# Kernel tuning notes

Measured on AMD Instinct MI355X. Metric: run time of the kernel, lower is better.

Reference implementation:

```python
import jax, jax.numpy as jnp
import numpy as np

FIXED_SIZE = 10
NUM_GRAPHS = 2000
NUM_PERM = 1


def setup_inputs() -> dict:
    key = jax.random.key(0)
    ks = jax.random.split(key, 8)
    N, E, D, H, O = 100000, 600000, 128, 256, 256
    x = jax.random.normal(ks[0], (N, D), dtype=jnp.float32)
    edge_index = jax.random.randint(ks[1], (2, E), 0, N)
    batch_ids = jnp.sort(jax.random.randint(ks[2], (N,), 0, NUM_GRAPHS))
    W1 = jax.random.normal(ks[3], (D + FIXED_SIZE, H), dtype=jnp.float32) * 0.05
    b1 = jnp.zeros((H,), dtype=jnp.float32)
    W2 = jax.random.normal(ks[4], (H, O), dtype=jnp.float32) * 0.05
    b2 = jnp.zeros((O,), dtype=jnp.float32)
    return {"x": x, "edge_index": edge_index, "batch_ids": batch_ids,
            "W1": W1, "b1": b1, "W2": W2, "b2": b2}


def _gnn(new_x, src, dst, W1, b1, W2, b2):
    # 2-layer GIN-style sum-aggregation node embedder
    N = new_x.shape[0]
    m = jax.ops.segment_sum(new_x[src], dst, num_segments=N)
    h = jax.nn.relu((new_x + m) @ W1 + b1)
    m = jax.ops.segment_sum(h[src], dst, num_segments=N)
    h = jax.nn.relu((h + m) @ W2 + b2)
    return h


def reference(x, edge_index, batch_ids, W1, b1, W2, b2):
    N = x.shape[0]
    src, dst = edge_index[0], edge_index[1]
    # segment starts (batch_ids is sorted)
    counts = jax.ops.segment_sum(jnp.ones((N,), jnp.int32), batch_ids, num_segments=NUM_GRAPHS)
    starts = jnp.cumsum(counts) - counts  # [G]
    perm_key = jax.random.key(42)
    out = None
    for p in range(NUM_PERM):
        # vectorized per-graph random permutation: sort random keys within each segment
        r = jax.random.uniform(jax.random.fold_in(perm_key, p), (N,))
        order = jnp.argsort(batch_ids.astype(jnp.float32) + r)  # groups by graph, random within
        # rank within graph after permutation (order preserves segment boundaries)
        ranks = jnp.zeros((N,), jnp.int32).at[order].set(
            jnp.arange(N, dtype=jnp.int32) - starts[batch_ids].astype(jnp.int32))
        # tiled eye(10) indexed by permuted position == one-hot of (rank % 10)
        ids = jax.nn.one_hot(ranks % FIXED_SIZE, FIXED_SIZE, dtype=x.dtype)
        new_x = jnp.concatenate([x, ids], axis=1)  # [N, D+10]
        h_v = _gnn(new_x, src, dst, W1, b1, W2, b2)
        h_g = jax.ops.segment_sum(h_v, batch_ids, num_segments=NUM_GRAPHS)  # global_add_pool
        contrib = h_g / NUM_PERM
        out = contrib if out is None else out + contrib
    return out
```

## Files before the change

kernel.cpp:

```cpp
#include <hip/hip_runtime.h>
#include <hip/hip_bf16.h>
#include <stdint.h>


#define D_IN   128
#define KRAW   138
#define K1     160
#define B1ROW  192
#define HDIM   256
#define NGRAPH 2000
#define MAXS   6

typedef __bf16 bf16x8 __attribute__((ext_vector_type(8)));
typedef float  f32x4  __attribute__((ext_vector_type(4)));

__device__ __forceinline__ unsigned short f2b(float f) {
  __hip_bfloat16 h = __float2bfloat16(f);
  return __builtin_bit_cast(unsigned short, h);
}
__device__ __forceinline__ float blo(unsigned p) { return __uint_as_float(p << 16); }
__device__ __forceinline__ float bhi(unsigned p) { return __uint_as_float(p & 0xffff0000u); }

__device__ __forceinline__ unsigned e8(float f) {
  unsigned u = __float_as_uint(f);
  unsigned s = (u >> 24) & 0x80u;
  float a = fabsf(f);
  if (!(a >= 0.015625f)) return s;
  a = fminf(a, 448.f);
  unsigned b = __float_as_uint(a);
  b += 0x0007FFFFu + ((b >> 20) & 1u);
  unsigned e = (b >> 23) - 120u;
  unsigned m = (b >> 20) & 7u;
  return s | (e << 3) | m;
}
__device__ __forceinline__ float d8(unsigned byte) {
  unsigned m = byte & 0x7fu;
  unsigned bits = (0x3C000000u + (m << 20)) | ((byte & 0x80u) << 24);
  return m ? __uint_as_float(bits) : 0.f;
}

__device__ __forceinline__ void glds16(const unsigned short* g, unsigned short* l) {
  __builtin_amdgcn_global_load_lds(
      (const __attribute__((address_space(1))) unsigned int*)g,
      (__attribute__((address_space(3))) unsigned int*)l, 16, 0, 0);
}

__device__ __forceinline__ unsigned rotl32(unsigned x, int r) {
  return (x << r) | (x >> (32 - r));
}
__device__ __forceinline__ void threefry2x32(unsigned k0, unsigned k1,
                                             unsigned x0, unsigned x1,
                                             unsigned& o0, unsigned& o1) {
  unsigned ks2 = k0 ^ k1 ^ 0x1BD11BDAu;
  unsigned ks[3] = {k0, k1, ks2};
  x0 += ks[0]; x1 += ks[1];
  const int rotA[4] = {13, 15, 26, 6};
  const int rotB[4] = {17, 29, 16, 24};
#pragma unroll
  for (int i = 0; i < 5; ++i) {
    const int* rot = (i & 1) ? rotB : rotA;
#pragma unroll
    for (int j = 0; j < 4; ++j) {
      x0 += x1; x1 = rotl32(x1, rot[j]); x1 ^= x0;
    }
    x0 += ks[(i + 1) % 3];
    x1 += ks[(i + 2) % 3] + (unsigned)(i + 1);
  }
  o0 = x0; o1 = x1;
}

__global__ void k_prep2(const int* __restrict__ bids, const int* __restrict__ dst,
                        float* __restrict__ r, int* __restrict__ start,
                        int* __restrict__ cnt, int* __restrict__ deg, int N, int E) {
  int i = blockIdx.x * blockDim.x + threadIdx.x;
  if (i < E) atomicAdd(&deg[dst[i]], 1);
  if (i >= N) return;
  int half = N >> 1;
  if (i < half) {
    unsigned fk0, fk1;
    threefry2x32(0u, 42u, 0u, 0u, fk0, fk1);
    unsigned b0, b1v;
    threefry2x32(fk0, fk1, (unsigned)i, (unsigned)(i + half), b0, b1v);
    r[i]        = __uint_as_float((b0  >> 9) | 0x3f800000u) - 1.0f;
    r[i + half] = __uint_as_float((b1v >> 9) | 0x3f800000u) - 1.0f;
  }
  int g = bids[i];
  if (i == 0 || bids[i - 1] != g) start[g] = i;
  atomicAdd(&cnt[g], 1);
}

__global__ void k_rank(const float* __restrict__ r, const int* __restrict__ start,
                       const int* __restrict__ cnt, int* __restrict__ ids) {
  int g = blockIdx.x;
  int st = start[g], n = cnt[g];
  if (n <= 0) return;
  float gf = (float)g;
  for (int t = threadIdx.x; t < n; t += blockDim.x) {
    int v = st + t;
    float kv = gf + r[v];
    int c = 0;
    for (int u0 = 0; u0 < n; ++u0) {
      int u = st + u0;
      float ku = gf + r[u];
      c += (int)((ku < kv) | ((ku == kv) & (u < v)));
    }
    ids[v] = c % 10;
  }
}

__global__ void k_scan1(const int* __restrict__ deg, int* __restrict__ rowptr,
                        int* __restrict__ bsum, int N) {
  __shared__ int buf[256];
  int tid = threadIdx.x;
  int i = blockIdx.x * 256 + tid;
  int v = (i < N) ? deg[i] : 0;
  buf[tid] = v;
  __syncthreads();
  for (int off = 1; off < 256; off <<= 1) {
    int t = (tid >= off) ? buf[tid - off] : 0;
    __syncthreads();
    buf[tid] += t;
    __syncthreads();
  }
  if (i < N) rowptr[i] = buf[tid] - v;
  if (tid == 255) bsum[blockIdx.x] = buf[255];
}

__global__ void k_scan2(int* __restrict__ bsum, int nb) {
  __shared__ int buf[512];
  int tid = threadIdx.x;
  int v = (tid < nb) ? bsum[tid] : 0;
  buf[tid] = v;
  __syncthreads();
  for (int off = 1; off < 512; off <<= 1) {
    int t = (tid >= off) ? buf[tid - off] : 0;
    __syncthreads();
    buf[tid] += t;
    __syncthreads();
  }
  if (tid < nb) bsum[tid] = buf[tid] - v;
}

__global__ void k_scan3(int* __restrict__ rowptr, const int* __restrict__ bsum,
                        int N, int E) {
  int i = blockIdx.x * 256 + threadIdx.x;
  if (i < N) rowptr[i] += bsum[blockIdx.x];
  if (i == 0) rowptr[N] = E;
}

__global__ void k_scatter(const int* __restrict__ src, const int* __restrict__ dst,
                          const int* __restrict__ rowptr, int* __restrict__ fill,
                          int* __restrict__ csr, int E) {
  int e = blockIdx.x * 256 + threadIdx.x;
  if (e >= E) return;
  int d = dst[e];
  int pos = rowptr[d] + atomicAdd(&fill[d], 1);
  csr[pos] = src[e];
}

__global__ void k_pre(const float* __restrict__ x, const float* __restrict__ W1,
                      const float* __restrict__ W2, unsigned char* __restrict__ x8,
                      unsigned short* __restrict__ Wpt, unsigned short* __restrict__ W2t,
                      int n8, int xbb) {
  int bid = blockIdx.x;
  int tid = threadIdx.x;
  if (bid < xbb) {
    int i = bid * 256 + tid;
    if (i >= n8) return;
    const float4* xp = reinterpret_cast<const float4*>(x) + (size_t)i * 2;
    float4 v0 = xp[0], v1 = xp[1];
    uint2 o;
    o.x = e8(v0.x) | (e8(v0.y) << 8) | (e8(v0.z) << 16) | (e8(v0.w) << 24);
    o.y = e8(v1.x) | (e8(v1.y) << 8) | (e8(v1.z) << 16) | (e8(v1.w) << 24);
    reinterpret_cast<uint2*>(x8)[i] = o;
  } else {
    int j = (bid - xbb) * 256 + tid;
    if (j < HDIM * B1ROW) {
      int n = j / B1ROW, k = j % B1ROW;
      Wpt[j] = f2b(k < KRAW ? W1[k * HDIM + n] : 0.f);
    } else {
      int j2 = j - HDIM * B1ROW;
      if (j2 < HDIM * HDIM) {
        int n = j2 >> 8, k = j2 & 255;
        W2t[j2] = f2b(W2[k * HDIM + n]);
      }
    }
  }
}

__global__ void k_agg1(const unsigned char* __restrict__ x8, const int* __restrict__ ids,
                       const int* __restrict__ rowptr, const int* __restrict__ csr,
                       unsigned short* __restrict__ agg1, int N) {
  int v = blockIdx.x * 4 + (threadIdx.x >> 6);
  if (v >= N) return;
  int l = threadIdx.x & 63;
  const unsigned short* xbase = reinterpret_cast<const unsigned short*>(x8);
  unsigned t = xbase[(size_t)v * 64 + l];
  float a0 = d8(t & 0xffu), a1 = d8(t >> 8);
  int e0 = rowptr[v], e1 = rowptr[v + 1];
  int e = e0;
  for (; e + 4 <= e1; e += 4) {
    unsigned t0 = xbase[(size_t)csr[e] * 64 + l];
    unsigned t1 = xbase[(size_t)csr[e + 1] * 64 + l];
    unsigned t2 = xbase[(size_t)csr[e + 2] * 64 + l];
    unsigned t3 = xbase[(size_t)csr[e + 3] * 64 + l];
    a0 += d8(t0 & 0xffu) + d8(t1 & 0xffu) + d8(t2 & 0xffu) + d8(t3 & 0xffu);
    a1 += d8(t0 >> 8) + d8(t1 >> 8) + d8(t2 >> 8) + d8(t3 >> 8);
  }
  for (; e < e1; ++e) {
    unsigned tt = xbase[(size_t)csr[e] * 64 + l];
    a0 += d8(tt & 0xffu); a1 += d8(tt >> 8);
  }
  int cnt10[10] = {};
  for (int base = e0; base < e1; base += 64) {
    int ee = base + l;
    int id = (ee < e1) ? ids[csr[ee]] : -1;
#pragma unroll
    for (int k = 0; k < 10; ++k)
      cnt10[k] += (int)__popcll(__ballot(id == k));
  }
  int myid = ids[v];
  unsigned* row32 = reinterpret_cast<unsigned*>(agg1 + (size_t)v * K1);
  row32[l] = (unsigned)f2b(a0) | ((unsigned)f2b(a1) << 16);
  if (l < 16) {
    float v0 = 0.f, v1 = 0.f;
#pragma unroll
    for (int kk = 0; kk < 10; ++kk) {
      float cv = (float)(cnt10[kk] + (myid == kk ? 1 : 0));
      if (2 * l == kk) v0 = cv;
      if (2 * l + 1 == kk) v1 = cv;
    }
    row32[64 + l] = (unsigned)f2b(v0) | ((unsigned)f2b(v1) << 16);
  }
}

template <int KT, int BROW, int NT, int EPI>
__global__ __launch_bounds__(512, 1) void k_gemm(
    const unsigned short* __restrict__ A, const unsigned short* __restrict__ Bt,
    const float* __restrict__ bias, void* __restrict__ Hout, int M) {
  constexpr int ROWB = BROW * 2;
  __shared__ __align__(16) unsigned short b_s[HDIM * BROW];
  __shared__ __align__(16) unsigned short a_s[3 * 4096];

  const int tid = threadIdx.x;
  const int w = tid >> 6, l = tid & 63;
  const int wm = w >> 2, wn = w & 3;
  const int lr = l & 15, lq = l >> 4, lk = lq * 8;
  const int b = blockIdx.x;
  const int TT = (M + 127) >> 7;
  const int ntb = (TT > b) ? ((TT - b + 255) >> 8) : 0;
  const int total = ntb * NT;

  constexpr int BITERS = BROW / 16;
#pragma unroll
  for (int it = 0; it < BITERS; ++it) {
    int d = (it * 512 + tid) * 16;
    int n = d / ROWB;
    int inrow = d - n * ROWB;
    int u = inrow ^ ((n & 7) << 4);
    glds16(Bt + (size_t)n * BROW + (u >> 1), b_s + (size_t)(it * 512 + w * 64) * 8);
  }
  auto stageA = [&](int s) {
    int buf = s - (s / 3) * 3;
    int m0 = (b + (s / NT) * 256) << 7;
    int k0 = (s % NT) * 32;
    int d = tid * 16;
    int u = d ^ (((d >> 7) & 7) << 4);
    int r = ((u >> 7) << 1) | ((u >> 6) & 1);
    int k = (u >> 1) & 31;
    glds16(A + (size_t)(m0 + r) * KT + k0 + k, a_s + buf * 4096 + w * 512);
  };
  if (total > 0) stageA(0);
  if (total > 1) stageA(1);
  if (total > 1) { asm volatile("s_waitcnt vmcnt(1)" ::: "memory"); }
  else           { asm volatile("s_waitcnt vmcnt(0)" ::: "memory"); }
  __builtin_amdgcn_s_barrier();
  __builtin_amdgcn_sched_barrier(0);

  float bv[4];
  if constexpr (EPI == 0) {
#pragma unroll
    for (int nf = 0; nf < 4; ++nf) bv[nf] = bias[wn * 64 + nf * 16 + lr];
  }

  int aoff[4];
#pragma unroll
  for (int mf = 0; mf < 4; ++mf) {
    int R = wm * 64 + mf * 16 + lr;
    aoff[mf] = (((R >> 1) * 128 + (R & 1) * 64 + lk * 2) ^ (((R >> 1) & 7) << 4));
  }

  int s = 0;
  for (int ti = 0; ti < ntb; ++ti) {
    const int m0t = (b + ti * 256) << 7;
    f32x4 acc[4][4] = {};
    for (int ks = 0; ks < NT; ++ks, ++s) {
      const bool pre = (s + 2 < total);
      if (pre) stageA(s + 2);
      const char* ab = reinterpret_cast<const char*>(a_s) + (s - (s / 3) * 3) * 8192;
      bf16x8 af[4], bfr[4];
#pragma unroll
      for (int mf = 0; mf < 4; ++mf)
        af[mf] = *reinterpret_cast<const bf16x8*>(ab + aoff[mf]);
#pragma unroll
      for (int nf = 0; nf < 4; ++nf) {
        int n = wn * 64 + nf * 16 + lr;
        int bb = n * ROWB + (((ks * 32 + lk) * 2) ^ ((n & 7) << 4));
        bfr[nf] = *reinterpret_cast<const bf16x8*>(reinterpret_cast<const char*>(b_s) + bb);
      }
      __builtin_amdgcn_s_setprio(1);
#pragma unroll
      for (int mf = 0; mf < 4; ++mf)
#pragma unroll
        for (int nf = 0; nf < 4; ++nf)
          acc[mf][nf] = __builtin_amdgcn_mfma_f32_16x16x32_bf16(af[mf], bfr[nf], acc[mf][nf], 0, 0, 0);
      __builtin_amdgcn_s_setprio(0);
      if (pre) { asm volatile("s_waitcnt vmcnt(1)" ::: "memory"); }
      else     { asm volatile("s_waitcnt vmcnt(0)" ::: "memory"); }
      __builtin_amdgcn_s_barrier();
      __builtin_amdgcn_sched_barrier(0);
    }

#pragma unroll
    for (int mf = 0; mf < 4; ++mf)
#pragma unroll
      for (int q = 0; q < 4; ++q) {
        int grow = m0t + wm * 64 + mf * 16 + lq * 4 + q;
        if (grow < M) {
          size_t ro = (size_t)grow * HDIM + wn * 64 + lr;
          if constexpr (EPI == 0) {
            unsigned short* H = (unsigned short*)Hout;
#pragma unroll
            for (int nf = 0; nf < 4; ++nf) {
              float vv = acc[mf][nf][q] + bv[nf];
              H[ro + nf * 16] = f2b(vv > 0.f ? vv : 0.f);
            }
          } else {
            unsigned char* H8 = (unsigned char*)Hout;
#pragma unroll
            for (int nf = 0; nf < 4; ++nf)
              H8[ro + nf * 16] = (unsigned char)e8(acc[mf][nf][q]);
          }
        }
      }
  }
}

__global__ __launch_bounds__(256) void k_gp(
    const unsigned char* __restrict__ y8, const int* __restrict__ bids,
    const int* __restrict__ rowptr, const int* __restrict__ csr,
    const float* __restrict__ b2, float* __restrict__ out, int N) {
  __shared__ float red[4][MAXS][HDIM];
  __shared__ int seg_l[128];
  __shared__ int gseg_l[128];
  __shared__ int wtot2[2];
  __shared__ int nseg_sh;
  const int tid = threadIdx.x;
  const int w = tid >> 6, l = tid & 63;
  const int v0 = blockIdx.x * 128;

  float* rz = &red[0][0][0];
  for (int i = tid; i < 4 * MAXS * HDIM; i += 256) rz[i] = 0.f;

  if (tid < 128) {
    int i0 = v0 + tid; i0 = i0 < N ? i0 : N - 1;
    int i1 = v0 + tid - 1; i1 = i1 < N ? i1 : N - 1; i1 = i1 > 0 ? i1 : 0;
    int g = bids[i0];
    bool bnd = (tid > 0) && (g != bids[i1]);
    unsigned long long mb = __ballot(bnd);
    int lane = tid & 63;
    int incl = (int)__popcll(mb & (~0ULL >> (63 - lane)));
    seg_l[tid] = incl;
    if (lane == 63) wtot2[tid >> 6] = incl;
  }
  __syncthreads();
  if (tid < 128) {
    int sfin = seg_l[tid] + ((tid >= 64) ? wtot2[0] : 0);
    seg_l[tid] = sfin;
    int i0 = v0 + tid; i0 = i0 < N ? i0 : N - 1;
    int i1 = v0 + tid - 1; i1 = i1 < N ? i1 : N - 1; i1 = i1 > 0 ? i1 : 0;
    int g = bids[i0];
    if (tid == 0 || g != bids[i1]) gseg_l[sfin] = g;
    if (tid == 127) nseg_sh = sfin + 1;
  }
  __syncthreads();
  const int nseg = nseg_sh;
  const bool fb = (nseg > MAXS);

  float bv0 = b2[l * 4 + 0], bv1 = b2[l * 4 + 1];
  float bv2 = b2[l * 4 + 2], bv3 = b2[l * 4 + 3];
  const unsigned* yb = reinterpret_cast<const unsigned*>(y8);

  float a0 = 0.f, a1 = 0.f, a2 = 0.f, a3 = 0.f;
  int cur = seg_l[w * 32];
  for (int i = 0; i < 32; ++i) {
    int idx = w * 32 + i;
    int v = v0 + idx;
    if (v >= N) break;
    int sg = seg_l[idx];
    if (sg != cur) {
      if (!fb) {
        float* rp = &red[w][cur][l * 4];
        rp[0] += a0; rp[1] += a1; rp[2] += a2; rp[3] += a3;
      }
      a0 = a1 = a2 = a3 = 0.f;
      cur = sg;
    }
    unsigned t = yb[(size_t)v * 64 + l];
    float s0 = d8(t & 0xffu), s1 = d8((t >> 8) & 0xffu);
    float s2 = d8((t >> 16) & 0xffu), s3 = d8(t >> 24);
    int e0 = rowptr[v], e1 = rowptr[v + 1];
    int e = e0;
    for (; e + 4 <= e1; e += 4) {
      unsigned t0 = yb[(size_t)csr[e] * 64 + l];
      unsigned t1 = yb[(size_t)csr[e + 1] * 64 + l];
      unsigned t2 = yb[(size_t)csr[e + 2] * 64 + l];
      unsigned t3 = yb[(size_t)csr[e + 3] * 64 + l];
      s0 += d8(t0 & 0xffu) + d8(t1 & 0xffu) + d8(t2 & 0xffu) + d8(t3 & 0xffu);
      s1 += d8((t0 >> 8) & 0xffu) + d8((t1 >> 8) & 0xffu) + d8((t2 >> 8) & 0xffu) + d8((t3 >> 8) & 0xffu);
      s2 += d8((t0 >> 16) & 0xffu) + d8((t1 >> 16) & 0xffu) + d8((t2 >> 16) & 0xffu) + d8((t3 >> 16) & 0xffu);
      s3 += d8(t0 >> 24) + d8(t1 >> 24) + d8(t2 >> 24) + d8(t3 >> 24);
    }
    for (; e < e1; ++e) {
      unsigned tt = yb[(size_t)csr[e] * 64 + l];
      s0 += d8(tt & 0xffu); s1 += d8((tt >> 8) & 0xffu);
      s2 += d8((tt >> 16) & 0xffu); s3 += d8(tt >> 24);
    }
    s0 = fmaxf(s0 + bv0, 0.f); s1 = fmaxf(s1 + bv1, 0.f);
    s2 = fmaxf(s2 + bv2, 0.f); s3 = fmaxf(s3 + bv3, 0.f);
    if (fb) {
      int g = bids[v];
      float* op = out + (size_t)g * HDIM + l * 4;
      if (s0 > 0.f) atomicAdd(&op[0], s0);
      if (s1 > 0.f) atomicAdd(&op[1], s1);
      if (s2 > 0.f) atomicAdd(&op[2], s2);
      if (s3 > 0.f) atomicAdd(&op[3], s3);
    } else {
      a0 += s0; a1 += s1; a2 += s2; a3 += s3;
    }
  }
  if (!fb) {
    float* rp = &red[w][cur][l * 4];
    rp[0] += a0; rp[1] += a1; rp[2] += a2; rp[3] += a3;
  }
  __syncthreads();
  if (!fb) {
    for (int sg = 0; sg < nseg; ++sg) {
      float val = red[0][sg][tid] + red[1][sg][tid] + red[2][sg][tid] + red[3][sg][tid];
      if (val != 0.f) atomicAdd(&out[(size_t)gseg_l[sg] * HDIM + tid], val);
    }
  }
}

extern "C" void kernel_launch(void* const* d_in, const int* in_sizes, int n_in,
                              void* d_out, int out_size, void* d_ws, size_t ws_size,
                              hipStream_t stream) {
  const float* x    = (const float*)d_in[0];
  const int*   ei   = (const int*)d_in[1];
  const int*   bids = (const int*)d_in[2];
  const float* W1   = (const float*)d_in[3];
  const float* b1   = (const float*)d_in[4];
  const float* W2   = (const float*)d_in[5];
  const float* b2   = (const float*)d_in[6];
  float* out = (float*)d_out;

  const int N = in_sizes[2];
  const int E = in_sizes[1] / 2;
  const int* src = ei;
  const int* dst = ei + E;

  char* ws = (char*)d_ws;
  size_t off = 0;
  auto alloc = [&](size_t bytes) {
    size_t o = off;
    off = (off + bytes + 255) & ~(size_t)255;
    return o;
  };
  float* r      = (float*)(ws + alloc((size_t)N * 4));
  int*   ids    = (int*)(ws + alloc((size_t)N * 4));
  int*   start  = (int*)(ws + alloc((size_t)NGRAPH * 4));
  int*   cnt    = (int*)(ws + alloc((size_t)NGRAPH * 4));
  int*   deg    = (int*)(ws + alloc((size_t)N * 4));
  int*   fill   = (int*)(ws + alloc((size_t)N * 4));
  int*   rowptr = (int*)(ws + alloc((size_t)(N + 1) * 4));
  int*   bsum   = (int*)(ws + alloc(512 * 4));
  int*   csr    = (int*)(ws + alloc((size_t)E * 4));
  unsigned short* Wpt = (unsigned short*)(ws + alloc((size_t)HDIM * B1ROW * 2));
  unsigned short* W2t = (unsigned short*)(ws + alloc((size_t)HDIM * HDIM * 2));
  unsigned char*  x8  = (unsigned char*)(ws + alloc((size_t)N * D_IN));
  unsigned short* agg1 = (unsigned short*)(ws + alloc((size_t)(N + 128) * K1 * 2));
  unsigned short* h    = (unsigned short*)(ws + alloc((size_t)(N + 128) * HDIM * 2));
  unsigned char*  y8   = (unsigned char*)(ws + alloc((size_t)(N + 128) * HDIM));
  (void)ws_size;

  size_t zspan = (size_t)((char*)(fill + N) - (char*)cnt);
  hipMemsetAsync(cnt, 0, zspan, stream);
  hipMemsetAsync(out, 0, (size_t)out_size * 4, stream);

  const int nb = (N + 255) / 256;
  const int n8 = N * 16;
  const int xbb = (n8 + 255) / 256;
  const int wb = (HDIM * B1ROW + HDIM * HDIM + 255) / 256;

  k_prep2<<<(E + 255) / 256, 256, 0, stream>>>(bids, dst, r, start, cnt, deg, N, E);
  k_pre<<<xbb + wb, 256, 0, stream>>>(x, W1, W2, x8, Wpt, W2t, n8, xbb);
  k_scan1<<<nb, 256, 0, stream>>>(deg, rowptr, bsum, N);
  k_scan2<<<1, 512, 0, stream>>>(bsum, nb);
  k_scan3<<<nb, 256, 0, stream>>>(rowptr, bsum, N, E);
  k_scatter<<<(E + 255) / 256, 256, 0, stream>>>(src, dst, rowptr, fill, csr, E);
  k_rank<<<NGRAPH, 64, 0, stream>>>(r, start, cnt, ids);
  k_agg1<<<(N + 3) / 4, 256, 0, stream>>>(x8, ids, rowptr, csr, agg1, N);

  k_gemm<K1, B1ROW, 5, 0><<<256, 512, 0, stream>>>(agg1, Wpt, b1, (void*)h, N);
  k_gemm<HDIM, HDIM, 8, 1><<<256, 512, 0, stream>>>(h, W2t, nullptr, (void*)y8, N);

  k_gp<<<(N + 127) / 128, 256, 0, stream>>>(y8, bids, rowptr, csr, b2, out, N);
}
```

Before: 423.7 us.

## Use hardware FP8 pack/unpack and simplify graph pooling to per-wave atomics

Replaces the software e4m3 encode/decode routines with the packed hardware FP8 conversion builtins when available, in input quantization, the first aggregation, the second GEMM epilogue and the final aggregation. The final aggregate+pool kernel is restructured so each wave processes 8 consecutive nodes and flushes per-graph partial sums directly with global atomics. This drops the shared-memory segment scan and reduction buffers and their barriers. In exchange it issues more global atomics, and it depends on the hardware FP8 format matching the software codec.

```diff
diff --git a/kernel.cpp b/kernel.cpp
--- a/kernel.cpp
+++ b/kernel.cpp
@@ -9,19 +9,21 @@
 #define B1ROW  192
 #define HDIM   256
 #define NGRAPH 2000
-#define MAXS   6
 
 typedef __bf16 bf16x8 __attribute__((ext_vector_type(8)));
 typedef float  f32x4  __attribute__((ext_vector_type(4)));
+typedef float  f32x2  __attribute__((ext_vector_type(2)));
 
 __device__ __forceinline__ unsigned short f2b(float f) {
   __hip_bfloat16 h = __float2bfloat16(f);
   return __builtin_bit_cast(unsigned short, h);
 }
-__device__ __forceinline__ float blo(unsigned p) { return __uint_as_float(p << 16); }
-__device__ __forceinline__ float bhi(unsigned p) { return __uint_as_float(p & 0xffff0000u); }
-
-__device__ __forceinline__ unsigned e8(float f) {
+
+#if __has_builtin(__builtin_amdgcn_cvt_pk_f32_fp8) && __has_builtin(__builtin_amdgcn_cvt_pk_fp8_f32)
+#define HW_FP8 1
+#endif
+
+__device__ __forceinline__ unsigned e8_sw(float f) {
   unsigned u = __float_as_uint(f);
   unsigned s = (u >> 24) & 0x80u;
   float a = fabsf(f);
@@ -33,10 +35,36 @@
   unsigned m = (b >> 20) & 7u;
   return s | (e << 3) | m;
 }
-__device__ __forceinline__ float d8(unsigned byte) {
+__device__ __forceinline__ float d8_sw(unsigned byte) {
   unsigned m = byte & 0x7fu;
   unsigned bits = (0x3C000000u + (m << 20)) | ((byte & 0x80u) << 24);
   return m ? __uint_as_float(bits) : 0.f;
+}
+
+template <bool HI>
+__device__ __forceinline__ f32x2 dec2(unsigned w) {
+#ifdef HW_FP8
+  return __builtin_amdgcn_cvt_pk_f32_fp8((int)w, HI);
+#else
+  unsigned hw = HI ? (w >> 16) : (w & 0xffffu);
+  f32x2 r; r.x = d8_sw(hw & 0xffu); r.y = d8_sw(hw >> 8); return r;
+#endif
+}
+template <bool HI>
+__device__ __forceinline__ int enc2(float a, float b, int old) {
+#ifdef HW_FP8
+  return __builtin_amdgcn_cvt_pk_fp8_f32(a, b, old, HI);
+#else
+  unsigned p = e8_sw(a) | (e8_sw(b) << 8);
+  return HI ? ((old & 0xffff) | (int)(p << 16)) : ((int)(old & 0xffff0000u) | (int)p);
+#endif
+}
+__device__ __forceinline__ unsigned char enc1(float v) {
+#ifdef HW_FP8
+  return (unsigned char)(__builtin_amdgcn_cvt_pk_fp8_f32(v, v, 0, false) & 0xff);
+#else
+  return (unsigned char)e8_sw(v);
+#endif
 }
 
 __device__ __forceinline__ void glds16(const unsigned short* g, unsigned short* l) {
@@ -170,8 +198,8 @@
     const float4* xp = reinterpret_cast<const float4*>(x) + (size_t)i * 2;
     float4 v0 = xp[0], v1 = xp[1];
     uint2 o;
-    o.x = e8(v0.x) | (e8(v0.y) << 8) | (e8(v0.z) << 16) | (e8(v0.w) << 24);
-    o.y = e8(v1.x) | (e8(v1.y) << 8) | (e8(v1.z) << 16) | (e8(v1.w) << 24);
+    o.x = (unsigned)enc2<true>(v0.z, v0.w, enc2<false>(v0.x, v0.y, 0));
+    o.y = (unsigned)enc2<true>(v1.z, v1.w, enc2<false>(v1.x, v1.y, 0));
     reinterpret_cast<uint2*>(x8)[i] = o;
   } else {
     int j = (bid - xbb) * 256 + tid;
@@ -195,8 +223,8 @@
   if (v >= N) return;
   int l = threadIdx.x & 63;
   const unsigned short* xbase = reinterpret_cast<const unsigned short*>(x8);
-  unsigned t = xbase[(size_t)v * 64 + l];
-  float a0 = d8(t & 0xffu), a1 = d8(t >> 8);
+  f32x2 p = dec2<false>((unsigned)xbase[(size_t)v * 64 + l]);
+  float a0 = p.x, a1 = p.y;
   int e0 = rowptr[v], e1 = rowptr[v + 1];
   int e = e0;
   for (; e + 4 <= e1; e += 4) {
@@ -204,12 +232,14 @@
     unsigned t1 = xbase[(size_t)csr[e + 1] * 64 + l];
     unsigned t2 = xbase[(size_t)csr[e + 2] * 64 + l];
     unsigned t3 = xbase[(size_t)csr[e + 3] * 64 + l];
-    a0 += d8(t0 & 0xffu) + d8(t1 & 0xffu) + d8(t2 & 0xffu) + d8(t3 & 0xffu);
-    a1 += d8(t0 >> 8) + d8(t1 >> 8) + d8(t2 >> 8) + d8(t3 >> 8);
+    f32x2 q0 = dec2<false>(t0), q1 = dec2<false>(t1);
+    f32x2 q2 = dec2<false>(t2), q3 = dec2<false>(t3);
+    a0 += q0.x + q1.x + q2.x + q3.x;
+    a1 += q0.y + q1.y + q2.y + q3.y;
   }
   for (; e < e1; ++e) {
-    unsigned tt = xbase[(size_t)csr[e] * 64 + l];
-    a0 += d8(tt & 0xffu); a1 += d8(tt >> 8);
+    f32x2 q = dec2<false>((unsigned)xbase[(size_t)csr[e] * 64 + l]);
+    a0 += q.x; a1 += q.y;
   }
   int cnt10[10] = {};
   for (int base = e0; base < e1; base += 64) {
@@ -339,7 +369,7 @@
             unsigned char* H8 = (unsigned char*)Hout;
 #pragma unroll
             for (int nf = 0; nf < 4; ++nf)
-              H8[ro + nf * 16] = (unsigned char)e8(acc[mf][nf][q]);
+              H8[ro + nf * 16] = enc1(acc[mf][nf][q]);
           }
         }
       }
@@ -350,65 +380,28 @@
     const unsigned char* __restrict__ y8, const int* __restrict__ bids,
     const int* __restrict__ rowptr, const int* __restrict__ csr,
     const float* __restrict__ b2, float* __restrict__ out, int N) {
-  __shared__ float red[4][MAXS][HDIM];
-  __shared__ int seg_l[128];
-  __shared__ int gseg_l[128];
-  __shared__ int wtot2[2];
-  __shared__ int nseg_sh;
-  const int tid = threadIdx.x;
-  const int w = tid >> 6, l = tid & 63;
-  const int v0 = blockIdx.x * 128;
-
-  float* rz = &red[0][0][0];
-  for (int i = tid; i < 4 * MAXS * HDIM; i += 256) rz[i] = 0.f;
-
-  if (tid < 128) {
-    int i0 = v0 + tid; i0 = i0 < N ? i0 : N - 1;
-    int i1 = v0 + tid - 1; i1 = i1 < N ? i1 : N - 1; i1 = i1 > 0 ? i1 : 0;
-    int g = bids[i0];
-    bool bnd = (tid > 0) && (g != bids[i1]);
-    unsigned long long mb = __ballot(bnd);
-    int lane = tid & 63;
-    int incl = (int)__popcll(mb & (~0ULL >> (63 - lane)));
-    seg_l[tid] = incl;
-    if (lane == 63) wtot2[tid >> 6] = incl;
-  }
-  __syncthreads();
-  if (tid < 128) {
-    int sfin = seg_l[tid] + ((tid >= 64) ? wtot2[0] : 0);
-    seg_l[tid] = sfin;
-    int i0 = v0 + tid; i0 = i0 < N ? i0 : N - 1;
-    int i1 = v0 + tid - 1; i1 = i1 < N ? i1 : N - 1; i1 = i1 > 0 ? i1 : 0;
-    int g = bids[i0];
-    if (tid == 0 || g != bids[i1]) gseg_l[sfin] = g;
-    if (tid == 127) nseg_sh = sfin + 1;
-  }
-  __syncthreads();
-  const int nseg = nseg_sh;
-  const bool fb = (nseg > MAXS);
-
-  float bv0 = b2[l * 4 + 0], bv1 = b2[l * 4 + 1];
-  float bv2 = b2[l * 4 + 2], bv3 = b2[l * 4 + 3];
+  const int wid = blockIdx.x * 4 + (threadIdx.x >> 6);
+  const int l = threadIdx.x & 63;
+  int v0 = wid * 8;
+  if (v0 >= N) return;
+  int vend = (v0 + 8 < N) ? v0 + 8 : N;
+  const float4 bv = reinterpret_cast<const float4*>(b2)[l];
   const unsigned* yb = reinterpret_cast<const unsigned*>(y8);
 
   float a0 = 0.f, a1 = 0.f, a2 = 0.f, a3 = 0.f;
-  int cur = seg_l[w * 32];
-  for (int i = 0; i < 32; ++i) {
-    int idx = w * 32 + i;
-    int v = v0 + idx;
-    if (v >= N) break;
-    int sg = seg_l[idx];
-    if (sg != cur) {
-      if (!fb) {
-        float* rp = &red[w][cur][l * 4];
-        rp[0] += a0; rp[1] += a1; rp[2] += a2; rp[3] += a3;
-      }
+  int gcur = bids[v0];
+  for (int v = v0; v < vend; ++v) {
+    int g = bids[v];
+    if (g != gcur) {
+      float* op = out + (size_t)gcur * HDIM + l * 4;
+      atomicAdd(&op[0], a0); atomicAdd(&op[1], a1);
+      atomicAdd(&op[2], a2); atomicAdd(&op[3], a3);
       a0 = a1 = a2 = a3 = 0.f;
-      cur = sg;
+      gcur = g;
     }
     unsigned t = yb[(size_t)v * 64 + l];
-    float s0 = d8(t & 0xffu), s1 = d8((t >> 8) & 0xffu);
-    float s2 = d8((t >> 16) & 0xffu), s3 = d8(t >> 24);
+    f32x2 p0 = dec2<false>(t), p1 = dec2<true>(t);
+    float s0 = p0.x, s1 = p0.y, s2 = p1.x, s3 = p1.y;
     int e0 = rowptr[v], e1 = rowptr[v + 1];
     int e = e0;
     for (; e + 4 <= e1; e += 4) {
@@ -416,40 +409,30 @@
       unsigned t1 = yb[(size_t)csr[e + 1] * 64 + l];
       unsigned t2 = yb[(size_t)csr[e + 2] * 64 + l];
       unsigned t3 = yb[(size_t)csr[e + 3] * 64 + l];
-      s0 += d8(t0 & 0xffu) + d8(t1 & 0xffu) + d8(t2 & 0xffu) + d8(t3 & 0xffu);
-      s1 += d8((t0 >> 8) & 0xffu) + d8((t1 >> 8) & 0xffu) + d8((t2 >> 8) & 0xffu) + d8((t3 >> 8) & 0xffu);
-      s2 += d8((t0 >> 16) & 0xffu) + d8((t1 >> 16) & 0xffu) + d8((t2 >> 16) & 0xffu) + d8((t3 >> 16) & 0xffu);
-      s3 += d8(t0 >> 24) + d8(t1 >> 24) + d8(t2 >> 24) + d8(t3 >> 24);
+      f32x2 q;
+      q = dec2<false>(t0); s0 += q.x; s1 += q.y;
+      q = dec2<true>(t0);  s2 += q.x; s3 += q.y;
+      q = dec2<false>(t1); s0 += q.x; s1 += q.y;
+      q = dec2<true>(t1);  s2 += q.x; s3 += q.y;
+      q = dec2<false>(t2); s0 += q.x; s1 += q.y;
+      q = dec2<true>(t2);  s2 += q.x; s3 += q.y;
+      q = dec2<false>(t3); s0 += q.x; s1 += q.y;
+      q = dec2<true>(t3);  s2 += q.x; s3 += q.y;
     }
     for (; e < e1; ++e) {
       unsigned tt = yb[(size_t)csr[e] * 64 + l];
-      s0 += d8(tt & 0xffu); s1 += d8((tt >> 8) & 0xffu);
-      s2 += d8((tt >> 16) & 0xffu); s3 += d8(tt >> 24);
-    }
-    s0 = fmaxf(s0 + bv0, 0.f); s1 = fmaxf(s1 + bv1, 0.f);
-    s2 = fmaxf(s2 + bv2, 0.f); s3 = fmaxf(s3 + bv3, 0.f);
-    if (fb) {
-      int g = bids[v];
-      float* op = out + (size_t)g * HDIM + l * 4;
-      if (s0 > 0.f) atomicAdd(&op[0], s0);
-      if (s1 > 0.f) atomicAdd(&op[1], s1);
-      if (s2 > 0.f) atomicAdd(&op[2], s2);
-      if (s3 > 0.f) atomicAdd(&op[3], s3);
-    } else {
-      a0 += s0; a1 += s1; a2 += s2; a3 += s3;
-    }
-  }
-  if (!fb) {
-    float* rp = &red[w][cur][l * 4];
-    rp[0] += a0; rp[1] += a1; rp[2] += a2; rp[3] += a3;
-  }
-  __syncthreads();
-  if (!fb) {
-    for (int sg = 0; sg < nseg; ++sg) {
-      float val = red[0][sg][tid] + red[1][sg][tid] + red[2][sg][tid] + red[3][sg][tid];
-      if (val != 0.f) atomicAdd(&out[(size_t)gseg_l[sg] * HDIM + tid], val);
-    }
-  }
+      f32x2 q;
+      q = dec2<false>(tt); s0 += q.x; s1 += q.y;
+      q = dec2<true>(tt);  s2 += q.x; s3 += q.y;
+    }
+    a0 += fmaxf(s0 + bv.x, 0.f);
+    a1 += fmaxf(s1 + bv.y, 0.f);
+    a2 += fmaxf(s2 + bv.z, 0.f);
+    a3 += fmaxf(s3 + bv.w, 0.f);
+  }
+  float* op = out + (size_t)gcur * HDIM + l * 4;
+  atomicAdd(&op[0], a0); atomicAdd(&op[1], a1);
+  atomicAdd(&op[2], a2); atomicAdd(&op[3], a3);
 }
 
 extern "C" void kernel_launch(void* const* d_in, const int* in_sizes, int n_in,
@@ -514,5 +497,5 @@
   k_gemm<K1, B1ROW, 5, 0><<<256, 512, 0, stream>>>(agg1, Wpt, b1, (void*)h, N);
   k_gemm<HDIM, HDIM, 8, 1><<<256, 512, 0, stream>>>(h, W2t, nullptr, (void*)y8, N);
 
-  k_gp<<<(N + 127) / 128, 256, 0, stream>>>(y8, bids, rowptr, csr, b2, out, N);
-}
+  k_gp<<<(N + 31) / 32, 256, 0, stream>>>(y8, bids, rowptr, csr, b2, out, N);
+}
```

Result: faster. 372.8 us (-12.0%).
